# Optimization experiments

Measured on AMD Instinct MI355X. Metric: run time of the kernel, lower is better.

The kernel has to match this reference:

```python
import jax, jax.numpy as jnp
import numpy as np

B, L, C = 4, 2048, 1024

def setup_inputs() -> dict:
    key = jax.random.key(0)
    k1, k2, k3 = jax.random.split(key, 3)
    net_in = jax.random.normal(k1, (B, L, C), dtype=jnp.float32)
    # torch Linear weights stored as (out, in); we keep that convention
    w_qkv = jax.random.normal(k2, (3 * C, C), dtype=jnp.float32) * (1.0 / np.sqrt(C))
    w_out = jax.random.normal(k3, (C, C), dtype=jnp.float32) * (1.0 / np.sqrt(C))
    return {"net_in": net_in, "w_qkv": w_qkv, "w_out": w_out}

def reference(net_in, w_qkv, w_out):
    Bc, Lc, Cc = net_in.shape
    qkv = jnp.einsum('blc,dc->bld', net_in, w_qkv)  # (B, L, 3C)
    q, k, v = jnp.split(qkv, 3, axis=-1)
    attn = jnp.einsum('bqc,bkc->bqk', q, k) / jnp.sqrt(jnp.float32(Cc))
    causal = jnp.tril(jnp.ones((Lc, Lc), dtype=bool))
    attn = jnp.where(causal[None, :, :], attn, -jnp.inf)
    attn = jax.nn.softmax(attn, axis=-1)
    out = jnp.einsum('bqk,bkc->bqc', attn, v)
    return jnp.einsum('blc,dc->bld', out, w_out)
```

## Files before the change

kernel.cpp:

```cpp
#include <hip/hip_runtime.h>
#include <hip/hip_bf16.h>
#include <cstdint>
#include <cstddef>

typedef __hip_bfloat16 bf16;
typedef float  floatx4 __attribute__((ext_vector_type(4)));
typedef __bf16 bf16x8  __attribute__((ext_vector_type(8)));

typedef __attribute__((address_space(1))) void as1_void;
typedef __attribute__((address_space(3))) void as3_void;

constexpr int Bn = 4, Ln = 2048, Cn = 1024;

__device__ __forceinline__ void store_one(float* p, float v) { *p = v; }
__device__ __forceinline__ void store_one(bf16*  p, float v) { *p = __float2bfloat16(v); }

template <typename OutT>
__device__ __forceinline__ void gemm_core(
    const bf16* __restrict__ A, const bf16* __restrict__ B, OutT* __restrict__ C,
    int m0, int n0, int Keff, int lda, int ldb, int ldc, float cscale)
{
    __shared__ __align__(16) bf16 smem[2 * 128 * 32];

    const int tid  = threadIdx.x;
    const int lane = tid & 63;
    const int quad = lane >> 4;
    const int lr   = lane & 15;
    const int wave = tid >> 6;
    const int wm   = (wave >> 1) * 64;
    const int wn   = (wave & 1) * 64;

    floatx4 acc[4][4];
#pragma unroll
    for (int i = 0; i < 4; ++i)
#pragma unroll
        for (int j = 0; j < 4; ++j) { floatx4 z = {0.f, 0.f, 0.f, 0.f}; acc[i][j] = z; }

    const bf16* gbase[4];
    int ldsoff[4];
#pragma unroll
    for (int it = 0; it < 4; ++it) {
        int chunk = it * 256 + tid;
        ldsoff[it] = __builtin_amdgcn_readfirstlane((chunk & ~63) * 16);
        int kc = chunk & 3;
        if (chunk < 512) {
            int m = chunk >> 2;
            gbase[it] = A + (size_t)(m0 + m) * lda + kc * 8;
        } else {
            int c2 = chunk - 512;
            int n = c2 >> 2;
            gbase[it] = B + (size_t)(n0 + n) * ldb + kc * 8;
        }
    }

    for (int k0 = 0; k0 < Keff; k0 += 32) {
        __syncthreads();
#pragma unroll
        for (int it = 0; it < 4; ++it) {
            uintptr_t ga = (uintptr_t)(gbase[it] + k0);
            uintptr_t la = (uintptr_t)((char*)smem + ldsoff[it]);
            __builtin_amdgcn_global_load_lds((const as1_void*)ga, (as3_void*)la, 16, 0, 0);
        }
        __syncthreads();

        const bf16* As = smem;
        const bf16* Bs = smem + 128 * 32;
        bf16x8 afrag[4], bfrag[4];
#pragma unroll
        for (int i = 0; i < 4; ++i)
            afrag[i] = *(const bf16x8*)(As + (size_t)(wm + i * 16 + lr) * 32 + quad * 8);
#pragma unroll
        for (int j = 0; j < 4; ++j)
            bfrag[j] = *(const bf16x8*)(Bs + (size_t)(wn + j * 16 + lr) * 32 + quad * 8);
#pragma unroll
        for (int i = 0; i < 4; ++i)
#pragma unroll
            for (int j = 0; j < 4; ++j)
                acc[i][j] = __builtin_amdgcn_mfma_f32_16x16x32_bf16(afrag[i], bfrag[j], acc[i][j], 0, 0, 0);
    }

#pragma unroll
    for (int i = 0; i < 4; ++i) {
        int row = m0 + wm + i * 16 + quad * 4;
#pragma unroll
        for (int j = 0; j < 4; ++j) {
            int col = n0 + wn + j * 16 + lr;
            OutT* cp = C + (size_t)row * ldc + col;
#pragma unroll
            for (int r = 0; r < 4; ++r)
                store_one(cp + (size_t)r * ldc, acc[i][j][r] * cscale);
        }
    }
}

__global__ __launch_bounds__(256)
void g1_w2_qk(const bf16* __restrict__ Xb, const bf16* __restrict__ Wqkb,
              const bf16* __restrict__ Wob, const bf16* __restrict__ WvT,
              bf16* __restrict__ QK, bf16* __restrict__ W2)
{
    int i = blockIdx.x;
    if (i < 64) {
        int m0 = (i & 7) * 128, n0 = (i >> 3) * 128;
        gemm_core<bf16>(Wob, WvT, W2, m0, n0, 1024, 1024, 1024, 1024, 1.0f);
    } else {
        int j = i - 64;
        int m0 = (j & 63) * 128, n0 = (j >> 6) * 128;
        gemm_core<bf16>(Xb, Wqkb, QK, m0, n0, 1024, 1024, 1024, 2048, 1.0f);
    }
}

__global__ __launch_bounds__(256)
void g2_vwt_s(const bf16* __restrict__ W2, const bf16* __restrict__ Xb,
              const bf16* __restrict__ QK, bf16* __restrict__ VWT,
              bf16* __restrict__ S)
{
    int i = blockIdx.x;
    if (i < 512) {
        int m0 = (i >> 6) * 128, n0 = (i & 63) * 128;
        gemm_core<bf16>(W2, Xb, VWT, m0, n0, 1024, 1024, 1024, 8192, 1.0f);
    } else {
        int s = i - 512;
        int b = (s & 7) >> 1;
        int p = s & 1;
        int t = (s >> 3) * 2 + p;
        int ti = (int)((sqrtf(8.f * t + 1.f) - 1.f) * 0.5f);
        while ((ti + 1) * (ti + 2) / 2 <= t) ++ti;
        while (ti * (ti + 1) / 2 > t) --ti;
        int tj = t - ti * (ti + 1) / 2;
        const bf16* Aq = QK + (long long)b * Ln * 2048;
        const bf16* Bk = Aq + 1024;
        bf16* Sb = S + (long long)b * Ln * Ln;
        gemm_core<bf16>(Aq, Bk, Sb, ti * 128, tj * 128, 1024, 2048, 2048, Ln, 0.03125f);
    }
}

__global__ __launch_bounds__(256)
void g3_out(const bf16* __restrict__ P, const bf16* __restrict__ VWT,
            float* __restrict__ out)
{
    int i = blockIdx.x;
    int r = i & 7, q = i >> 3;
    int b = r >> 1, p = r & 1;
    int mt = 15 - (q >> 2), nt = p + 2 * (q & 3);
    int m0 = mt * 128, n0 = nt * 128;
    const bf16* Pp = P + (long long)b * Ln * Ln;
    const bf16* Bv = VWT + b * Ln;
    float* Co = out + (long long)b * Ln * Cn;
    gemm_core<float>(Pp, Bv, Co, m0, n0, m0 + 128, Ln, 8192, Cn, 1.0f);
}

__device__ __forceinline__ float waveMax(float x) {
#pragma unroll
    for (int o = 32; o > 0; o >>= 1) x = fmaxf(x, __shfl_xor(x, o, 64));
    return x;
}
__device__ __forceinline__ float waveSum(float x) {
#pragma unroll
    for (int o = 32; o > 0; o >>= 1) x += __shfl_xor(x, o, 64);
    return x;
}

__global__ __launch_bounds__(256)
void softmax_causal(bf16* __restrict__ S)
{
    const int wave = threadIdx.x >> 6, lane = threadIdx.x & 63;
    const int row = blockIdx.x * 4 + wave;
    const int q = row & (Ln - 1);
    bf16* Srow = S + (long long)row * Ln;
    const int kmax = ((q >> 7) + 1) << 7;
    const int nv = (kmax + 511) >> 9;

    float x[4][8];
    float m = -1e30f;
    for (int it = 0; it < nv; ++it) {
        int c0 = it * 512 + lane * 8;
        bf16x8 v = *(const bf16x8*)(Srow + c0);
#pragma unroll
        for (int e = 0; e < 8; ++e) {
            float f = (float)v[e];
            f = (c0 + e <= q) ? f : -1e30f;
            x[it][e] = f;
            m = fmaxf(m, f);
        }
    }
    m = waveMax(m);
    float s = 0.f;
    for (int it = 0; it < nv; ++it)
#pragma unroll
        for (int e = 0; e < 8; ++e) {
            float ex = (x[it][e] > -1e29f) ? __expf(x[it][e] - m) : 0.f;
            x[it][e] = ex;
            s += ex;
        }
    s = waveSum(s);
    float inv = 1.f / s;
    for (int it = 0; it < nv; ++it) {
        bf16x8 o;
#pragma unroll
        for (int e = 0; e < 8; ++e) o[e] = (__bf16)(x[it][e] * inv);
        *(bf16x8*)(Srow + it * 512 + lane * 8) = o;
    }
}

__global__ __launch_bounds__(256)
void cast_all(const float* __restrict__ X, const float* __restrict__ Wqkv,
              const float* __restrict__ Wo,
              bf16* __restrict__ Xb, bf16* __restrict__ Wqkb,
              bf16* __restrict__ Wob, bf16* __restrict__ WvT)
{
    int blk = blockIdx.x;
    if (blk < 11264) {
        int i = blk * 256 + threadIdx.x;
        const float* src; bf16* dst; int off;
        if (i < 2097152)                 { src = X;    dst = Xb;   off = i; }
        else if (i < 2097152 + 524288)   { src = Wqkv; dst = Wqkb; off = i - 2097152; }
        else                             { src = Wo;   dst = Wob;  off = i - 2621440; }
        float4 f = ((const float4*)src)[off];
        bf16 o0 = __float2bfloat16(f.x), o1 = __float2bfloat16(f.y);
        bf16 o2 = __float2bfloat16(f.z), o3 = __float2bfloat16(f.w);
        ushort4 u;
        u.x = *(unsigned short*)&o0; u.y = *(unsigned short*)&o1;
        u.z = *(unsigned short*)&o2; u.w = *(unsigned short*)&o3;
        *(ushort4*)(dst + (size_t)off * 4) = u;
    } else {
        __shared__ float t[32][33];
        int tt = blk - 11264;
        int c0 = (tt & 31) * 32;
        int r0 = (tt >> 5) * 32;
        const float* Wv = Wqkv + 2048 * 1024;
        int xcol = threadIdx.x & 31, y0 = threadIdx.x >> 5;
#pragma unroll
        for (int p = 0; p < 4; ++p) {
            int y = y0 + 8 * p;
            t[y][xcol] = Wv[(size_t)(r0 + y) * 1024 + c0 + xcol];
        }
        __syncthreads();
#pragma unroll
        for (int p = 0; p < 4; ++p) {
            int mloc = y0 + 8 * p;
            WvT[(size_t)(c0 + mloc) * 1024 + r0 + xcol] = __float2bfloat16(t[xcol][mloc]);
        }
    }
}

extern "C" void kernel_launch(void* const* d_in, const int* in_sizes, int n_in,
                              void* d_out, int out_size, void* d_ws, size_t ws_size,
                              hipStream_t stream)
{
    const float* X    = (const float*)d_in[0];
    const float* Wqkv = (const float*)d_in[1];
    const float* Wout = (const float*)d_in[2];
    float* out = (float*)d_out;

    char* ws = (char*)d_ws;
    const size_t MiB = 1024ull * 1024ull;
    bf16* Xb   = (bf16*)(ws + 0);
    bf16* QK   = (bf16*)(ws + 16 * MiB);
    bf16* VWT  = (bf16*)(ws + 48 * MiB);
    bf16* Sbuf = (bf16*)(ws + 64 * MiB);
    bf16* Wqkb = (bf16*)(ws + 96 * MiB);
    bf16* WvT  = (bf16*)(ws + 100 * MiB);
    bf16* Wob  = (bf16*)(ws + 102 * MiB);
    bf16* W2   = (bf16*)(ws + 104 * MiB);

    cast_all<<<dim3(12288), 256, 0, stream>>>(X, Wqkv, Wout, Xb, Wqkb, Wob, WvT);

    g1_w2_qk<<<dim3(1088), 256, 0, stream>>>(Xb, Wqkb, Wob, WvT, QK, W2);

    g2_vwt_s<<<dim3(1056), 256, 0, stream>>>(W2, Xb, QK, VWT, Sbuf);

    softmax_causal<<<dim3(Bn * Ln / 4), 256, 0, stream>>>(Sbuf);

    g3_out<<<dim3(512), 256, 0, stream>>>(Sbuf, VWT, out);
}
```

Baseline: 248.8 us.

## Use 256x256 double-buffered GEMM tiles and fuse softmax into VWT launch

Replaces the 128x128 single-buffered GEMM core with a 256x256 tile, 512-thread kernel. It uses a K=64 double-buffered LDS pipeline with swizzled layout, split barriers, and MFMA priority raising. The kernel stages are regrouped: QK projection alone, then S plus W2, then VWT fused with the causal softmax in one launch, then the output GEMM. The aim is more data reuse per tile, overlap of global loads with MFMA, and fewer launches. The cost is fewer blocks, coarser causal tile granularity and heavy LDS use per block.

```diff
diff --git a/kernel.cpp b/kernel.cpp
--- a/kernel.cpp
+++ b/kernel.cpp
@@ -15,138 +15,176 @@
 __device__ __forceinline__ void store_one(float* p, float v) { *p = v; }
 __device__ __forceinline__ void store_one(bf16*  p, float v) { *p = __float2bfloat16(v); }
 
+#define BAR()    asm volatile("s_barrier" ::: "memory")
+#define VMCNT2() asm volatile("s_waitcnt vmcnt(2)" ::: "memory")
+#define VMCNT0() asm volatile("s_waitcnt vmcnt(0)" ::: "memory")
+#define SCHEDB() __builtin_amdgcn_sched_barrier(0)
+#define STAGE(gp, off) \
+    __builtin_amdgcn_global_load_lds((const as1_void*)(gp), (as3_void*)(smem + (off)), 16, 0, 0)
+
 template <typename OutT>
-__device__ __forceinline__ void gemm_core(
+__device__ __forceinline__ void gemm256(
     const bf16* __restrict__ A, const bf16* __restrict__ B, OutT* __restrict__ C,
     int m0, int n0, int Keff, int lda, int ldb, int ldc, float cscale)
 {
-    __shared__ __align__(16) bf16 smem[2 * 128 * 32];
+    __shared__ __align__(16) char smem[131072];
 
     const int tid  = threadIdx.x;
     const int lane = tid & 63;
     const int quad = lane >> 4;
     const int lr   = lane & 15;
     const int wave = tid >> 6;
-    const int wm   = (wave >> 1) * 64;
-    const int wn   = (wave & 1) * 64;
-
-    floatx4 acc[4][4];
-#pragma unroll
-    for (int i = 0; i < 4; ++i)
+    const int wm   = (wave >> 2) * 128;
+    const int wn   = (wave & 3) * 64;
+
+    floatx4 acc[8][4];
+#pragma unroll
+    for (int i = 0; i < 8; ++i)
 #pragma unroll
         for (int j = 0; j < 4; ++j) { floatx4 z = {0.f, 0.f, 0.f, 0.f}; acc[i][j] = z; }
 
-    const bf16* gbase[4];
-    int ldsoff[4];
-#pragma unroll
-    for (int it = 0; it < 4; ++it) {
-        int chunk = it * 256 + tid;
-        ldsoff[it] = __builtin_amdgcn_readfirstlane((chunk & ~63) * 16);
-        int kc = chunk & 3;
-        if (chunk < 512) {
-            int m = chunk >> 2;
-            gbase[it] = A + (size_t)(m0 + m) * lda + kc * 8;
-        } else {
-            int c2 = chunk - 512;
-            int n = c2 >> 2;
-            gbase[it] = B + (size_t)(n0 + n) * ldb + kc * 8;
-        }
-    }
-
-    for (int k0 = 0; k0 < Keff; k0 += 32) {
-        __syncthreads();
-#pragma unroll
-        for (int it = 0; it < 4; ++it) {
-            uintptr_t ga = (uintptr_t)(gbase[it] + k0);
-            uintptr_t la = (uintptr_t)((char*)smem + ldsoff[it]);
-            __builtin_amdgcn_global_load_lds((const as1_void*)ga, (as3_void*)la, 16, 0, 0);
-        }
-        __syncthreads();
-
-        const bf16* As = smem;
-        const bf16* Bs = smem + 128 * 32;
-        bf16x8 afrag[4], bfrag[4];
-#pragma unroll
-        for (int i = 0; i < 4; ++i)
-            afrag[i] = *(const bf16x8*)(As + (size_t)(wm + i * 16 + lr) * 32 + quad * 8);
-#pragma unroll
-        for (int j = 0; j < 4; ++j)
-            bfrag[j] = *(const bf16x8*)(Bs + (size_t)(wn + j * 16 + lr) * 32 + quad * 8);
-#pragma unroll
-        for (int i = 0; i < 4; ++i)
-#pragma unroll
-            for (int j = 0; j < 4; ++j)
-                acc[i][j] = __builtin_amdgcn_mfma_f32_16x16x32_bf16(afrag[i], bfrag[j], acc[i][j], 0, 0, 0);
-    }
-
-#pragma unroll
-    for (int i = 0; i < 4; ++i) {
-        int row = m0 + wm + i * 16 + quad * 4;
-#pragma unroll
-        for (int j = 0; j < 4; ++j) {
-            int col = n0 + wn + j * 16 + lr;
+    const int srow = tid >> 3;
+    const int sx   = (tid & 7) ^ (srow & 7);
+    const bf16* gA = A + (size_t)(m0 + srow) * lda + sx * 8;
+    const bf16* gB = B + (size_t)(n0 + srow) * ldb + sx * 8;
+    const int wuni = __builtin_amdgcn_readfirstlane((tid & 0x1C0) * 16);
+
+    const int aoff = (wm + lr) * 64;
+    const int boff = (wn + lr) * 64;
+    const int s0   = (quad ^ (lr & 7)) * 8;
+
+    const int NT = Keff >> 6;
+
+    STAGE(gB,            32768 + 0 * 8192 + wuni);
+    STAGE(gB + 64  * ldb, 32768 + 1 * 8192 + wuni);
+    STAGE(gB + 128 * ldb, 32768 + 2 * 8192 + wuni);
+    STAGE(gB + 192 * ldb, 32768 + 3 * 8192 + wuni);
+    STAGE(gA,                     0 * 8192 + wuni);
+    STAGE(gA + 128 * lda,         2 * 8192 + wuni);
+    STAGE(gA + 64  * lda,         1 * 8192 + wuni);
+    STAGE(gA + 192 * lda,         3 * 8192 + wuni);
+    VMCNT2();
+    BAR();
+
+#define LDA4(MB, SK) do { _Pragma("unroll") for (int ii = 0; ii < 4; ++ii) \
+        a[ii] = *(const bf16x8*)(As + aoff + ((MB) * 4 + ii) * 1024 + (SK)); } while (0)
+#define LDB4(SK) do { _Pragma("unroll") for (int nn = 0; nn < 4; ++nn) \
+        b[nn] = *(const bf16x8*)(Bs + boff + nn * 1024 + (SK)); } while (0)
+#define MFMA16(MB) do { _Pragma("unroll") for (int ii = 0; ii < 4; ++ii) { \
+        _Pragma("unroll") for (int nn = 0; nn < 4; ++nn) \
+            acc[(MB) * 4 + ii][nn] = __builtin_amdgcn_mfma_f32_16x16x32_bf16( \
+                a[ii], b[nn], acc[(MB) * 4 + ii][nn], 0, 0, 0); } } while (0)
+
+    for (int t = 0; t < NT; ++t) {
+        const bf16* As = (const bf16*)(smem + (t & 1) * 65536);
+        const bf16* Bs = (const bf16*)(smem + (t & 1) * 65536 + 32768);
+        const int  wl  = ((t + 1) & 1) * 65536;
+        const int  kn  = (t + 1) << 6;
+        const bool more = (t + 1 < NT);
+        bf16x8 a[4], b[4];
+
+        LDB4(s0);
+        LDA4(0, s0);
+        if (more) {
+            STAGE(gB + kn,            wl + 32768 + 0 * 8192 + wuni);
+            STAGE(gB + kn + 64 * ldb, wl + 32768 + 1 * 8192 + wuni);
+        }
+        BAR(); SCHEDB();
+        __builtin_amdgcn_s_setprio(1);
+        MFMA16(0);
+        __builtin_amdgcn_s_setprio(0);
+        SCHEDB();
+        if (more) VMCNT2(); else VMCNT0();
+        BAR();
+
+        LDA4(1, s0);
+        if (more) {
+            STAGE(gB + kn + 128 * ldb, wl + 32768 + 2 * 8192 + wuni);
+            STAGE(gB + kn + 192 * ldb, wl + 32768 + 3 * 8192 + wuni);
+        }
+        BAR(); SCHEDB();
+        __builtin_amdgcn_s_setprio(1);
+        MFMA16(1);
+        __builtin_amdgcn_s_setprio(0);
+        SCHEDB();
+        BAR();
+
+        LDB4(s0 ^ 32);
+        LDA4(0, s0 ^ 32);
+        if (more) {
+            STAGE(gA + kn,             wl + 0 * 8192 + wuni);
+            STAGE(gA + kn + 128 * lda, wl + 2 * 8192 + wuni);
+        }
+        BAR(); SCHEDB();
+        __builtin_amdgcn_s_setprio(1);
+        MFMA16(0);
+        __builtin_amdgcn_s_setprio(0);
+        SCHEDB();
+        BAR();
+
+        LDA4(1, s0 ^ 32);
+        if (more) {
+            STAGE(gA + kn + 64  * lda, wl + 1 * 8192 + wuni);
+            STAGE(gA + kn + 192 * lda, wl + 3 * 8192 + wuni);
+        }
+        BAR(); SCHEDB();
+        __builtin_amdgcn_s_setprio(1);
+        MFMA16(1);
+        __builtin_amdgcn_s_setprio(0);
+        SCHEDB();
+        if (more) VMCNT2();
+        BAR();
+    }
+#undef LDA4
+#undef LDB4
+#undef MFMA16
+
+#pragma unroll
+    for (int mi = 0; mi < 8; ++mi) {
+        const int row = m0 + wm + mi * 16 + quad * 4;
+#pragma unroll
+        for (int n = 0; n < 4; ++n) {
+            const int col = n0 + wn + n * 16 + lr;
             OutT* cp = C + (size_t)row * ldc + col;
 #pragma unroll
             for (int r = 0; r < 4; ++r)
-                store_one(cp + (size_t)r * ldc, acc[i][j][r] * cscale);
-        }
-    }
-}
-
-__global__ __launch_bounds__(256)
-void g1_w2_qk(const bf16* __restrict__ Xb, const bf16* __restrict__ Wqkb,
-              const bf16* __restrict__ Wob, const bf16* __restrict__ WvT,
-              bf16* __restrict__ QK, bf16* __restrict__ W2)
-{
-    int i = blockIdx.x;
-    if (i < 64) {
-        int m0 = (i & 7) * 128, n0 = (i >> 3) * 128;
-        gemm_core<bf16>(Wob, WvT, W2, m0, n0, 1024, 1024, 1024, 1024, 1.0f);
-    } else {
-        int j = i - 64;
-        int m0 = (j & 63) * 128, n0 = (j >> 6) * 128;
-        gemm_core<bf16>(Xb, Wqkb, QK, m0, n0, 1024, 1024, 1024, 2048, 1.0f);
-    }
-}
-
-__global__ __launch_bounds__(256)
-void g2_vwt_s(const bf16* __restrict__ W2, const bf16* __restrict__ Xb,
-              const bf16* __restrict__ QK, bf16* __restrict__ VWT,
-              bf16* __restrict__ S)
-{
-    int i = blockIdx.x;
-    if (i < 512) {
-        int m0 = (i >> 6) * 128, n0 = (i & 63) * 128;
-        gemm_core<bf16>(W2, Xb, VWT, m0, n0, 1024, 1024, 1024, 8192, 1.0f);
-    } else {
-        int s = i - 512;
-        int b = (s & 7) >> 1;
-        int p = s & 1;
-        int t = (s >> 3) * 2 + p;
+                store_one(cp + (size_t)r * ldc, acc[mi][n][r] * cscale);
+        }
+    }
+}
+
+__global__ __launch_bounds__(512, 2)
+void g1_qk(const bf16* __restrict__ Xb, const bf16* __restrict__ Wqkb,
+           bf16* __restrict__ QK)
+{
+    const int i = blockIdx.x;
+    const int j = i >> 3;
+    const int mt = (i & 7) * 4 + (j & 3);
+    const int nt = j >> 2;
+    gemm256<bf16>(Xb, Wqkb, QK, mt * 256, nt * 256, 1024, 1024, 1024, 2048, 1.0f);
+}
+
+__global__ __launch_bounds__(512, 2)
+void g2_s_w2(const bf16* __restrict__ QK, const bf16* __restrict__ Wob,
+             const bf16* __restrict__ WvT, bf16* __restrict__ S,
+             bf16* __restrict__ W2)
+{
+    const int i = blockIdx.x;
+    if (i < 144) {
+        const int b = (i & 7) >> 1;
+        const int t = (i >> 3) * 2 + (i & 1);
         int ti = (int)((sqrtf(8.f * t + 1.f) - 1.f) * 0.5f);
         while ((ti + 1) * (ti + 2) / 2 <= t) ++ti;
         while (ti * (ti + 1) / 2 > t) --ti;
-        int tj = t - ti * (ti + 1) / 2;
-        const bf16* Aq = QK + (long long)b * Ln * 2048;
+        const int tj = t - ti * (ti + 1) / 2;
+        const bf16* Aq = QK + (size_t)b * Ln * 2048;
         const bf16* Bk = Aq + 1024;
-        bf16* Sb = S + (long long)b * Ln * Ln;
-        gemm_core<bf16>(Aq, Bk, Sb, ti * 128, tj * 128, 1024, 2048, 2048, Ln, 0.03125f);
-    }
-}
-
-__global__ __launch_bounds__(256)
-void g3_out(const bf16* __restrict__ P, const bf16* __restrict__ VWT,
-            float* __restrict__ out)
-{
-    int i = blockIdx.x;
-    int r = i & 7, q = i >> 3;
-    int b = r >> 1, p = r & 1;
-    int mt = 15 - (q >> 2), nt = p + 2 * (q & 3);
-    int m0 = mt * 128, n0 = nt * 128;
-    const bf16* Pp = P + (long long)b * Ln * Ln;
-    const bf16* Bv = VWT + b * Ln;
-    float* Co = out + (long long)b * Ln * Cn;
-    gemm_core<float>(Pp, Bv, Co, m0, n0, m0 + 128, Ln, 8192, Cn, 1.0f);
+        bf16* Sb = S + (size_t)b * Ln * Ln;
+        gemm256<bf16>(Aq, Bk, Sb, ti * 256, tj * 256, 1024, 2048, 2048, Ln, 0.03125f);
+    } else {
+        const int j = i - 144;
+        gemm256<bf16>(Wob, WvT, W2, (j & 3) * 256, (j >> 2) * 256, 1024, 1024, 1024, 1024, 1.0f);
+    }
 }
 
 __device__ __forceinline__ float waveMax(float x) {
@@ -160,46 +198,75 @@
     return x;
 }
 
-__global__ __launch_bounds__(256)
-void softmax_causal(bf16* __restrict__ S)
+__device__ void softmax_rows(bf16* __restrict__ S, int row0)
 {
     const int wave = threadIdx.x >> 6, lane = threadIdx.x & 63;
-    const int row = blockIdx.x * 4 + wave;
-    const int q = row & (Ln - 1);
-    bf16* Srow = S + (long long)row * Ln;
-    const int kmax = ((q >> 7) + 1) << 7;
-    const int nv = (kmax + 511) >> 9;
-
-    float x[4][8];
-    float m = -1e30f;
-    for (int it = 0; it < nv; ++it) {
-        int c0 = it * 512 + lane * 8;
-        bf16x8 v = *(const bf16x8*)(Srow + c0);
-#pragma unroll
-        for (int e = 0; e < 8; ++e) {
-            float f = (float)v[e];
-            f = (c0 + e <= q) ? f : -1e30f;
-            x[it][e] = f;
-            m = fmaxf(m, f);
-        }
-    }
-    m = waveMax(m);
-    float s = 0.f;
-    for (int it = 0; it < nv; ++it)
-#pragma unroll
-        for (int e = 0; e < 8; ++e) {
-            float ex = (x[it][e] > -1e29f) ? __expf(x[it][e] - m) : 0.f;
-            x[it][e] = ex;
-            s += ex;
-        }
-    s = waveSum(s);
-    float inv = 1.f / s;
-    for (int it = 0; it < nv; ++it) {
-        bf16x8 o;
-#pragma unroll
-        for (int e = 0; e < 8; ++e) o[e] = (__bf16)(x[it][e] * inv);
-        *(bf16x8*)(Srow + it * 512 + lane * 8) = o;
-    }
+    for (int it8 = 0; it8 < 8; ++it8) {
+        const int row = row0 + wave * 8 + it8;
+        const int q = row & (Ln - 1);
+        bf16* Srow = S + (size_t)row * Ln;
+        const int kmax = ((q >> 7) + 1) << 7;
+        const int nv = (kmax + 511) >> 9;
+        float x[4][8];
+        float m = -1e30f;
+        for (int it = 0; it < nv; ++it) {
+            int c0 = it * 512 + lane * 8;
+            bf16x8 v = *(const bf16x8*)(Srow + c0);
+#pragma unroll
+            for (int e = 0; e < 8; ++e) {
+                float f = (float)v[e];
+                f = (c0 + e <= q) ? f : -1e30f;
+                x[it][e] = f;
+                m = fmaxf(m, f);
+            }
+        }
+        m = waveMax(m);
+        float s = 0.f;
+        for (int it = 0; it < nv; ++it)
+#pragma unroll
+            for (int e = 0; e < 8; ++e) {
+                float ex = (x[it][e] > -1e29f) ? __expf(x[it][e] - m) : 0.f;
+                x[it][e] = ex;
+                s += ex;
+            }
+        s = waveSum(s);
+        const float inv = 1.f / s;
+        for (int it = 0; it < nv; ++it) {
+            bf16x8 o;
+#pragma unroll
+            for (int e = 0; e < 8; ++e) o[e] = (__bf16)(x[it][e] * inv);
+            *(bf16x8*)(Srow + it * 512 + lane * 8) = o;
+        }
+    }
+}
+
+__global__ __launch_bounds__(512, 2)
+void g3_vwt_sm(const bf16* __restrict__ W2, const bf16* __restrict__ Xb,
+               bf16* __restrict__ VWT, bf16* __restrict__ S)
+{
+    const int i = blockIdx.x;
+    if (i < 128) {
+        const int j = i >> 3;
+        const int nt = (i & 7) * 4 + (j & 3);
+        const int mt = j >> 2;
+        gemm256<bf16>(W2, Xb, VWT, mt * 256, nt * 256, 1024, 1024, 1024, 8192, 1.0f);
+    } else {
+        softmax_rows(S, (i - 128) * 64);
+    }
+}
+
+__global__ __launch_bounds__(512, 2)
+void g4_out(const bf16* __restrict__ P, const bf16* __restrict__ VWT,
+            float* __restrict__ out)
+{
+    const int i = blockIdx.x;
+    const int b = (i & 7) >> 1, p = i & 1;
+    const int q = i >> 3;
+    const int mt = q >> 1, nt = p * 2 + (q & 1);
+    const bf16* Pp = P + (size_t)b * Ln * Ln;
+    const bf16* Bv = VWT + (size_t)b * Ln;
+    float* Co = out + (size_t)b * Ln * Cn;
+    gemm256<float>(Pp, Bv, Co, mt * 256, nt * 256, (mt + 1) * 256, Ln, 8192, Cn, 1.0f);
 }
 
 __global__ __launch_bounds__(256)
@@ -265,11 +332,11 @@
 
     cast_all<<<dim3(12288), 256, 0, stream>>>(X, Wqkv, Wout, Xb, Wqkb, Wob, WvT);
 
-    g1_w2_qk<<<dim3(1088), 256, 0, stream>>>(Xb, Wqkb, Wob, WvT, QK, W2);
-
-    g2_vwt_s<<<dim3(1056), 256, 0, stream>>>(W2, Xb, QK, VWT, Sbuf);
-
-    softmax_causal<<<dim3(Bn * Ln / 4), 256, 0, stream>>>(Sbuf);
-
-    g3_out<<<dim3(512), 256, 0, stream>>>(Sbuf, VWT, out);
-}
+    g1_qk<<<dim3(256), 512, 0, stream>>>(Xb, Wqkb, QK);
+
+    g2_s_w2<<<dim3(160), 512, 0, stream>>>(QK, Wob, WvT, Sbuf, W2);
+
+    g3_vwt_sm<<<dim3(256), 512, 0, stream>>>(W2, Xb, VWT, Sbuf);
+
+    g4_out<<<dim3(128), 512, 0, stream>>>(Sbuf, VWT, out);
+}
```

Result: faster. 239.8 us (-3.6%).
